# Performance work log

Measured on AMD Instinct MI355X. Metric: run time of the kernel, lower is better.

The kernel has to match this reference:

```python
import jax, jax.numpy as jnp
import numpy as np

N, F, H, C, HX, E = 50000, 256, 128, 16, 64, 500000
TEMP = 1.0


def gcn_conv(x, src, dst, W, b, n):
    # PyG GCNConv: x @ W, add self-loops, sym-normalized scatter-sum src->dst
    xw = x @ W
    idx = jnp.arange(n)
    s = jnp.concatenate([src, idx])
    d = jnp.concatenate([dst, idx])
    deg = jax.ops.segment_sum(jnp.ones_like(s, dtype=xw.dtype), d, num_segments=n)
    dinv = jnp.where(deg > 0, jax.lax.rsqrt(deg), 0.0)
    norm = dinv[s] * dinv[d]
    out = jax.ops.segment_sum(xw[s] * norm[:, None], d, num_segments=n)
    return out + b


def setup_inputs() -> dict:
    key = jax.random.key(0)
    ks = jax.random.split(key, 16)
    x = jax.random.normal(ks[0], (N, F), jnp.float32)
    edge_index = jax.random.randint(ks[1], (2, E), 0, N)
    neg_edge_index = jax.random.randint(ks[2], (2, E), 0, N)
    y = jax.random.randint(ks[3], (N,), 0, C)
    train_mask = jax.random.uniform(ks[4], (N,)) < 0.5
    def lin(k, fi, fo):
        s = 1.0 / np.sqrt(fi)
        return jax.random.uniform(k, (fi, fo), jnp.float32, -s, s)
    W1 = lin(ks[5], F, H); b1 = jnp.zeros((H,), jnp.float32)
    W2 = lin(ks[6], H, C); b2 = jnp.zeros((C,), jnp.float32)
    Wx = lin(ks[7], F, HX); bx = jnp.zeros((HX,), jnp.float32)
    Wd = lin(ks[8], 2 * (HX + C), 1); bd = jnp.zeros((1,), jnp.float32)
    return dict(x=x, edge_index=edge_index, neg_edge_index=neg_edge_index, y=y,
                train_mask=train_mask, W1=W1, b1=b1, W2=W2, b2=b2,
                Wx=Wx, bx=bx, Wd=Wd, bd=bd)


def reference(x, edge_index, neg_edge_index, y, train_mask,
              W1, b1, W2, b2, Wx, bx, Wd, bd):
    n = x.shape[0]
    # GNN encoder p(y|x,G): 2-layer GCN (eval mode -> dropout identity)
    h = jax.nn.relu(gcn_conv(x, edge_index[0], edge_index[1], W1, b1, n))
    logits = gcn_conv(h, edge_index[0], edge_index[1], W2, b2, n) / TEMP
    y_log_prob = jax.nn.log_softmax(logits, axis=-1)
    y_prob = jnp.where(train_mask[:, None],
                       jax.nn.one_hot(y, logits.shape[-1], dtype=logits.dtype),
                       jnp.exp(y_log_prob))
    # node feature encoder
    xe = jax.nn.relu(x @ Wx + bx)
    def decode(ei):
        s, d = ei[0], ei[1]
        feat = jnp.concatenate([xe[s], xe[d], y_prob[s], y_prob[d]], axis=1)
        return feat @ Wd + bd
    e_pred_pos = decode(edge_index)
    e_pred_neg = decode(neg_edge_index)
    return e_pred_pos, e_pred_neg, y_log_prob
```

## Files before the change

kernel.cpp:

```cpp
#include <hip/hip_runtime.h>

typedef unsigned short ushort_t;
typedef __attribute__((ext_vector_type(8))) short short8;
typedef __attribute__((ext_vector_type(4))) float floatx4;

constexpr int F = 256, H = 128, C = 16, HX = 64;
constexpr int NBCOL = H + HX;

__device__ __forceinline__ ushort_t f2bf(float f) {
  unsigned u = __float_as_uint(f);
  u += 0x7fffu + ((u >> 16) & 1u);
  return (ushort_t)(u >> 16);
}
__device__ __forceinline__ float bflo(unsigned u) { return __uint_as_float(u << 16); }
__device__ __forceinline__ float bfhi(unsigned u) { return __uint_as_float(u & 0xffff0000u); }

__global__ void k_pre(const float* __restrict__ x, ushort_t* __restrict__ xb, int total8,
                      const float* __restrict__ W1, const float* __restrict__ Wx,
                      ushort_t* __restrict__ WBt,
                      const int* __restrict__ dst, int* __restrict__ deg, int e,
                      int nbx, int nbw) {
  int b = blockIdx.x;
  if (b < nbx) {
    int i = b * 256 + threadIdx.x;
    if (i >= total8) return;
    const float4* xp = (const float4*)x;
    float4 a = xp[2 * i], bb = xp[2 * i + 1];
    ushort4 lo = make_ushort4(f2bf(a.x), f2bf(a.y), f2bf(a.z), f2bf(a.w));
    ushort4 hi = make_ushort4(f2bf(bb.x), f2bf(bb.y), f2bf(bb.z), f2bf(bb.w));
    ((ushort4*)xb)[2 * i] = lo;
    ((ushort4*)xb)[2 * i + 1] = hi;
  } else if (b < nbx + nbw) {
    int i = (b - nbx) * 256 + threadIdx.x;
    if (i >= NBCOL * F) return;
    int nn = i / F, k = i % F;
    float v = (nn < H) ? W1[k * H + nn] : Wx[k * HX + (nn - H)];
    WBt[nn * F + k] = f2bf(v);
  } else {
    int i = (b - nbx - nbw) * 256 + threadIdx.x;
    if (i < e) atomicAdd(&deg[dst[i]], 1);
  }
}

__global__ void k_scan_a(const int* __restrict__ deg, int* __restrict__ part, int n) {
  __shared__ int sm[256];
  int i = blockIdx.x * 256 + threadIdx.x;
  int v = (i < n) ? deg[i] : 0;
  sm[threadIdx.x] = v;
  __syncthreads();
  for (int s = 128; s > 0; s >>= 1) {
    if (threadIdx.x < s) sm[threadIdx.x] += sm[threadIdx.x + s];
    __syncthreads();
  }
  if (threadIdx.x == 0) part[blockIdx.x] = sm[0];
}

__global__ void k_scan_b(const int* __restrict__ part, int* __restrict__ blockoff, int nparts) {
  __shared__ int sm[256];
  int t = threadIdx.x;
  int v = (t < nparts) ? part[t] : 0;
  sm[t] = v;
  __syncthreads();
  for (int d = 1; d < 256; d <<= 1) {
    int add = (t >= d) ? sm[t - d] : 0;
    __syncthreads();
    sm[t] += add;
    __syncthreads();
  }
  blockoff[t] = sm[t] - v;
}

__global__ void k_scan_c(const int* __restrict__ deg, const int* __restrict__ blockoff,
                         int* __restrict__ row_start, int* __restrict__ cursor,
                         float* __restrict__ dinv, int n, int e) {
  int i = blockIdx.x * 256 + threadIdx.x;
  int lane = threadIdx.x & 63, wid = threadIdx.x >> 6;
  int v = (i < n) ? deg[i] : 0;
  int x = v;
  for (int d = 1; d < 64; d <<= 1) {
    int t = __shfl_up(x, d);
    if (lane >= d) x += t;
  }
  __shared__ int wsum[4], woff[4];
  if (lane == 63) wsum[wid] = x;
  __syncthreads();
  if (threadIdx.x == 0) {
    int s = 0;
    for (int w = 0; w < 4; w++) { woff[w] = s; s += wsum[w]; }
  }
  __syncthreads();
  int excl = x - v + woff[wid] + blockoff[blockIdx.x];
  if (i < n) {
    row_start[i] = excl;
    cursor[i] = excl;
    dinv[i] = rsqrtf((float)(v + 1));
  }
  if (i == 0) row_start[n] = e;
}

__global__ void k_fill(const int* __restrict__ src, const int* __restrict__ dst,
                       const float* __restrict__ dinv, int* __restrict__ cursor,
                       int2* __restrict__ csr8, int e) {
  int i = blockIdx.x * 256 + threadIdx.x;
  if (i < e) {
    int s = src[i];
    int p = atomicAdd(&cursor[dst[i]], 1);
    csr8[p] = make_int2(s, __float_as_int(dinv[s]));
  }
}

__global__ __launch_bounds__(256, 3) void k_gemm1(const ushort_t* __restrict__ xb,
                                                  const ushort_t* __restrict__ WBt,
                                                  const float* __restrict__ bx,
                                                  ushort_t* __restrict__ xw1,
                                                  float* __restrict__ xe,
                                                  int n, int ntiles) {
  int w = threadIdx.x >> 6, lane = threadIdx.x & 63;
  int q = lane >> 4, l15 = lane & 15;
  const short8* bb = (const short8*)WBt;
  short8 bfr[3][8];
#pragma unroll
  for (int t = 0; t < 3; t++)
#pragma unroll
    for (int kk = 0; kk < 8; kk++)
      bfr[t][kk] = bb[(size_t)(w * 48 + t * 16 + l15) * 32 + kk * 4 + q];

  float bxv[3];
#pragma unroll
  for (int t = 0; t < 3; t++) {
    int g = w * 48 + t * 16;
    bxv[t] = (g >= H) ? bx[g - H + l15] : 0.0f;
  }

  for (int tile = blockIdx.x; tile < ntiles; tile += gridDim.x) {
    int row = tile * 16 + l15;
    const short8* arow = (const short8*)(xb + (size_t)min(row, n - 1) * F);
    short8 a[8];
#pragma unroll
    for (int kk = 0; kk < 8; kk++) a[kk] = arow[kk * 4 + q];

    floatx4 acc0 = (floatx4)(0.0f), acc1 = (floatx4)(0.0f), acc2 = (floatx4)(0.0f);
#pragma unroll
    for (int kk = 0; kk < 8; kk++) {
      acc0 = __builtin_amdgcn_mfma_f32_16x16x32_bf16(a[kk], bfr[0][kk], acc0, 0, 0, 0);
      acc1 = __builtin_amdgcn_mfma_f32_16x16x32_bf16(a[kk], bfr[1][kk], acc1, 0, 0, 0);
      acc2 = __builtin_amdgcn_mfma_f32_16x16x32_bf16(a[kk], bfr[2][kk], acc2, 0, 0, 0);
    }

    floatx4 accs[3] = {acc0, acc1, acc2};
    int rbase = tile * 16 + q * 4;
#pragma unroll
    for (int t = 0; t < 3; t++) {
      int g = w * 48 + t * 16;
#pragma unroll
      for (int r = 0; r < 4; r++) {
        int ro = rbase + r;
        if (ro < n) {
          if (g < H) {
            xw1[(size_t)ro * H + g + l15] = f2bf(accs[t][r]);
          } else {
            xe[(size_t)ro * HX + (g - H) + l15] = fmaxf(accs[t][r] + bxv[t], 0.0f);
          }
        }
      }
    }
  }
}

__global__ void k_agg1g2(const ushort_t* __restrict__ xw1, const int* __restrict__ row_start,
                         const int2* __restrict__ csr8, const float* __restrict__ dinv,
                         const float* __restrict__ b1, const float* __restrict__ W2,
                         float* __restrict__ hw2, int n) {
  __shared__ float2 hsm[4][64];
  int wid = threadIdx.x >> 6;
  int v = blockIdx.x * 4 + wid;
  if (v >= n) return;
  int lane = threadIdx.x & 63;
  float dv = dinv[v];
  unsigned sv = ((const unsigned*)(xw1 + (size_t)v * H))[lane];
  float ax = dv * bflo(sv), ay = dv * bfhi(sv);
  int j0 = row_start[v], j1 = row_start[v + 1];
  int j = j0;
  for (; j + 8 <= j1; j += 8) {
    int2 ee[8];
    unsigned rr[8];
#pragma unroll
    for (int u = 0; u < 8; u++) ee[u] = csr8[j + u];
#pragma unroll
    for (int u = 0; u < 8; u++)
      rr[u] = ((const unsigned*)(xw1 + (size_t)ee[u].x * H))[lane];
#pragma unroll
    for (int u = 0; u < 8; u++) {
      float wu = __int_as_float(ee[u].y);
      ax += wu * bflo(rr[u]);
      ay += wu * bfhi(rr[u]);
    }
  }
  for (; j < j1; j++) {
    int2 e0 = csr8[j];
    unsigned r0 = ((const unsigned*)(xw1 + (size_t)e0.x * H))[lane];
    float w0 = __int_as_float(e0.y);
    ax += w0 * bflo(r0);
    ay += w0 * bfhi(r0);
  }
  int c2 = lane * 2;
  float o0 = fmaxf(dv * ax + b1[c2], 0.0f);
  float o1 = fmaxf(dv * ay + b1[c2 + 1], 0.0f);
  hsm[wid][lane] = make_float2(o0, o1);

  int c = lane & 15, g = lane >> 4;
  const float* hrow = (const float*)hsm[wid];
  float p = 0.0f;
#pragma unroll
  for (int jj = 0; jj < 32; jj++)
    p += hrow[g * 32 + jj] * W2[(g * 32 + jj) * C + c];
  p += __shfl_xor(p, 16);
  p += __shfl_xor(p, 32);
  if (g == 0) hw2[(size_t)v * C + c] = p;
}

__global__ void k_agg2ab(const float* __restrict__ hw2, const int* __restrict__ row_start,
                         const int2* __restrict__ csr8, const float* __restrict__ dinv,
                         const float* __restrict__ b2, const int* __restrict__ y,
                         const int* __restrict__ tmask, const float* __restrict__ xe,
                         const float* __restrict__ Wd, float* __restrict__ ylp_out,
                         float* __restrict__ Aarr, float* __restrict__ Barr, int n) {
  int idx = blockIdx.x * 256 + threadIdx.x;
  int node = idx >> 4, c = idx & 15;
  if (node >= n) return;
  float dv = dinv[node];
  float acc = dv * hw2[(size_t)node * C + c];
  int j0 = row_start[node], j1 = row_start[node + 1];
  int j = j0;
  for (; j + 8 <= j1; j += 8) {
    int2 ee[8];
    float rr[8];
#pragma unroll
    for (int u = 0; u < 8; u++) ee[u] = csr8[j + u];
#pragma unroll
    for (int u = 0; u < 8; u++) rr[u] = hw2[(size_t)ee[u].x * C + c];
#pragma unroll
    for (int u = 0; u < 8; u++) acc += __int_as_float(ee[u].y) * rr[u];
  }
  for (; j + 4 <= j1; j += 4) {
    int2 e0 = csr8[j], e1 = csr8[j + 1], e2 = csr8[j + 2], e3 = csr8[j + 3];
    float r0 = hw2[(size_t)e0.x * C + c];
    float r1 = hw2[(size_t)e1.x * C + c];
    float r2 = hw2[(size_t)e2.x * C + c];
    float r3 = hw2[(size_t)e3.x * C + c];
    acc += __int_as_float(e0.y) * r0 + __int_as_float(e1.y) * r1 +
           __int_as_float(e2.y) * r2 + __int_as_float(e3.y) * r3;
  }
  for (; j < j1; j++) {
    int2 e0 = csr8[j];
    acc += __int_as_float(e0.y) * hw2[(size_t)e0.x * C + c];
  }
  float logit = dv * acc + b2[c];
  float m = logit;
  for (int o = 8; o > 0; o >>= 1) m = fmaxf(m, __shfl_xor(m, o, 16));
  float e = expf(logit - m);
  float s16 = e;
  for (int o = 8; o > 0; o >>= 1) s16 += __shfl_xor(s16, o, 16);
  float lp = (logit - m) - logf(s16);
  ylp_out[(size_t)node * C + c] = lp;
  float yp = tmask[node] ? ((y[node] == c) ? 1.0f : 0.0f) : (e / s16);

  float4 xv = *(const float4*)(xe + (size_t)node * HX + c * 4);
  float4 wa = *(const float4*)(Wd + c * 4);
  float4 wb = *(const float4*)(Wd + HX + c * 4);
  float pa = xv.x * wa.x + xv.y * wa.y + xv.z * wa.z + xv.w * wa.w + yp * Wd[2 * HX + c];
  float pb = xv.x * wb.x + xv.y * wb.y + xv.z * wb.z + xv.w * wb.w + yp * Wd[2 * HX + C + c];
  for (int o = 8; o > 0; o >>= 1) {
    pa += __shfl_xor(pa, o, 16);
    pb += __shfl_xor(pb, o, 16);
  }
  if (c == 0) { Aarr[node] = pa; Barr[node] = pb; }
}

__global__ void k_decode(const int* __restrict__ ei, const int* __restrict__ nei,
                         const float* __restrict__ Aarr, const float* __restrict__ Barr,
                         const float* __restrict__ bd, float* __restrict__ out, int e) {
  int i = blockIdx.x * 256 + threadIdx.x;
  if (i >= 2 * e) return;
  float b0 = bd[0];
  if (i < e) {
    int s = ei[i], d = ei[e + i];
    out[i] = Aarr[s] + Barr[d] + b0;
  } else {
    int j = i - e;
    int s = nei[j], d = nei[e + j];
    out[e + j] = Aarr[s] + Barr[d] + b0;
  }
}

extern "C" void kernel_launch(void* const* d_in, const int* in_sizes, int n_in,
                              void* d_out, int out_size, void* d_ws, size_t ws_size,
                              hipStream_t stream) {
  const float* x = (const float*)d_in[0];
  const int* ei = (const int*)d_in[1];
  const int* nei = (const int*)d_in[2];
  const int* y = (const int*)d_in[3];
  const int* tmask = (const int*)d_in[4];
  const float* W1 = (const float*)d_in[5];
  const float* b1 = (const float*)d_in[6];
  const float* W2 = (const float*)d_in[7];
  const float* b2 = (const float*)d_in[8];
  const float* Wx = (const float*)d_in[9];
  const float* bx = (const float*)d_in[10];
  const float* Wd = (const float*)d_in[11];
  const float* bd = (const float*)d_in[12];
  float* out = (float*)d_out;

  int n = in_sizes[3];
  int e = in_sizes[1] / 2;

  char* ws = (char*)d_ws;
  size_t off = 0;
  auto alloc = [&](size_t bytes) -> void* {
    void* p = ws + off;
    off += (bytes + 511) & ~(size_t)511;
    return p;
  };
  int* deg = (int*)alloc((size_t)n * 4);
  ushort_t* xb = (ushort_t*)alloc((size_t)n * F * 2);
  ushort_t* WBt = (ushort_t*)alloc((size_t)NBCOL * F * 2);
  ushort_t* xw1 = (ushort_t*)alloc((size_t)n * H * 2);
  float* xe = (float*)alloc((size_t)n * HX * 4);
  float* hw2 = (float*)alloc((size_t)n * C * 4);
  float* dinv = (float*)alloc((size_t)n * 4);
  int* row_start = (int*)alloc((size_t)(n + 1) * 4);
  int* cursor = (int*)alloc((size_t)n * 4);
  int2* csr8 = (int2*)alloc((size_t)e * 8);
  int* part = (int*)alloc(1024 * 4);
  int* blockoff = (int*)alloc(1024 * 4);
  float* Aarr = (float*)alloc((size_t)n * 4);
  float* Barr = (float*)alloc((size_t)n * 4);

  const int* src = ei;
  const int* dst = ei + e;

  hipMemsetAsync(deg, 0, (size_t)n * 4, stream);

  int total8 = n * F / 8;
  int nbx = (total8 + 255) / 256;
  int nbw = (NBCOL * F + 255) / 256;
  int nbe = (e + 255) / 256;
  k_pre<<<nbx + nbw + nbe, 256, 0, stream>>>(x, xb, total8, W1, Wx, WBt, dst, deg, e,
                                             nbx, nbw);

  int nblk = (n + 255) / 256;
  k_scan_a<<<nblk, 256, 0, stream>>>(deg, part, n);
  k_scan_b<<<1, 256, 0, stream>>>(part, blockoff, nblk);
  k_scan_c<<<nblk, 256, 0, stream>>>(deg, blockoff, row_start, cursor, dinv, n, e);
  k_fill<<<(e + 255) / 256, 256, 0, stream>>>(src, dst, dinv, cursor, csr8, e);

  int ntiles = (n + 15) / 16;
  int ggrid = ntiles < 768 ? ntiles : 768;
  k_gemm1<<<ggrid, 256, 0, stream>>>(xb, WBt, bx, xw1, xe, n, ntiles);
  k_agg1g2<<<(n + 3) / 4, 256, 0, stream>>>(xw1, row_start, csr8, dinv, b1, W2, hw2, n);
  k_agg2ab<<<(n * 16 + 255) / 256, 256, 0, stream>>>(hw2, row_start, csr8, dinv, b2, y,
                                                     tmask, xe, Wd, out + (size_t)2 * e,
                                                     Aarr, Barr, n);
  k_decode<<<(2 * e + 255) / 256, 256, 0, stream>>>(ei, nei, Aarr, Barr, bd, out, e);
}
```

Before: 256.3 us.

## Split GEMM tiles across scan and fill kernels to overlap latency-bound stages

Splits the dense x@[W1|Wx] GEMM into four quarters and fuses each quarter into one of the CSR-building stages (block reduce, single-block scan, final scan, edge fill). Extra blocks in each launch run GEMM tiles while the small latency-bound scan and atomic fill blocks execute, so the GEMM hides their idle time. The fill kernel becomes grid-stride with a fixed block count. The cost is heavier launches with extra register-hungry GEMM blocks, which may slow the scan stages. The GEMM B-fragments are also reloaded four times.

```diff
diff --git a/kernel.cpp b/kernel.cpp
--- a/kernel.cpp
+++ b/kernel.cpp
@@ -6,6 +6,8 @@
 
 constexpr int F = 256, H = 128, C = 16, HX = 64;
 constexpr int NBCOL = H + HX;
+constexpr int GEMM_BLKS = 768;
+constexpr int FILL_BLKS = 512;
 
 __device__ __forceinline__ ushort_t f2bf(float f) {
   unsigned u = __float_as_uint(f);
@@ -42,79 +44,12 @@
   }
 }
 
-__global__ void k_scan_a(const int* __restrict__ deg, int* __restrict__ part, int n) {
-  __shared__ int sm[256];
-  int i = blockIdx.x * 256 + threadIdx.x;
-  int v = (i < n) ? deg[i] : 0;
-  sm[threadIdx.x] = v;
-  __syncthreads();
-  for (int s = 128; s > 0; s >>= 1) {
-    if (threadIdx.x < s) sm[threadIdx.x] += sm[threadIdx.x + s];
-    __syncthreads();
-  }
-  if (threadIdx.x == 0) part[blockIdx.x] = sm[0];
-}
-
-__global__ void k_scan_b(const int* __restrict__ part, int* __restrict__ blockoff, int nparts) {
-  __shared__ int sm[256];
-  int t = threadIdx.x;
-  int v = (t < nparts) ? part[t] : 0;
-  sm[t] = v;
-  __syncthreads();
-  for (int d = 1; d < 256; d <<= 1) {
-    int add = (t >= d) ? sm[t - d] : 0;
-    __syncthreads();
-    sm[t] += add;
-    __syncthreads();
-  }
-  blockoff[t] = sm[t] - v;
-}
-
-__global__ void k_scan_c(const int* __restrict__ deg, const int* __restrict__ blockoff,
-                         int* __restrict__ row_start, int* __restrict__ cursor,
-                         float* __restrict__ dinv, int n, int e) {
-  int i = blockIdx.x * 256 + threadIdx.x;
-  int lane = threadIdx.x & 63, wid = threadIdx.x >> 6;
-  int v = (i < n) ? deg[i] : 0;
-  int x = v;
-  for (int d = 1; d < 64; d <<= 1) {
-    int t = __shfl_up(x, d);
-    if (lane >= d) x += t;
-  }
-  __shared__ int wsum[4], woff[4];
-  if (lane == 63) wsum[wid] = x;
-  __syncthreads();
-  if (threadIdx.x == 0) {
-    int s = 0;
-    for (int w = 0; w < 4; w++) { woff[w] = s; s += wsum[w]; }
-  }
-  __syncthreads();
-  int excl = x - v + woff[wid] + blockoff[blockIdx.x];
-  if (i < n) {
-    row_start[i] = excl;
-    cursor[i] = excl;
-    dinv[i] = rsqrtf((float)(v + 1));
-  }
-  if (i == 0) row_start[n] = e;
-}
-
-__global__ void k_fill(const int* __restrict__ src, const int* __restrict__ dst,
-                       const float* __restrict__ dinv, int* __restrict__ cursor,
-                       int2* __restrict__ csr8, int e) {
-  int i = blockIdx.x * 256 + threadIdx.x;
-  if (i < e) {
-    int s = src[i];
-    int p = atomicAdd(&cursor[dst[i]], 1);
-    csr8[p] = make_int2(s, __float_as_int(dinv[s]));
-  }
-}
-
-__global__ __launch_bounds__(256, 3) void k_gemm1(const ushort_t* __restrict__ xb,
-                                                  const ushort_t* __restrict__ WBt,
-                                                  const float* __restrict__ bx,
-                                                  ushort_t* __restrict__ xw1,
-                                                  float* __restrict__ xe,
-                                                  int n, int ntiles) {
+__device__ __forceinline__ void gemm_tiles(const ushort_t* __restrict__ xb,
+                                           const ushort_t* __restrict__ WBt,
+                                           const float* __restrict__ bx,
+                                           ushort_t* __restrict__ xw1,
+                                           float* __restrict__ xe, int n,
+                                           int t0, int t1, int bidx, int nb) {
   int w = threadIdx.x >> 6, lane = threadIdx.x & 63;
   int q = lane >> 4, l15 = lane & 15;
   const short8* bb = (const short8*)WBt;
@@ -132,7 +67,7 @@
     bxv[t] = (g >= H) ? bx[g - H + l15] : 0.0f;
   }
 
-  for (int tile = blockIdx.x; tile < ntiles; tile += gridDim.x) {
+  for (int tile = t0 + bidx; tile < t1; tile += nb) {
     int row = tile * 16 + l15;
     const short8* arow = (const short8*)(xb + (size_t)min(row, n - 1) * F);
     short8 a[8];
@@ -165,6 +100,116 @@
       }
     }
   }
+}
+
+__global__ __launch_bounds__(256, 3) void k_s2(const int* __restrict__ deg,
+                                               int* __restrict__ part, int n, int nchunk,
+                                               const ushort_t* __restrict__ xb,
+                                               const ushort_t* __restrict__ WBt,
+                                               const float* __restrict__ bx,
+                                               ushort_t* __restrict__ xw1,
+                                               float* __restrict__ xe, int t0, int t1) {
+  if ((int)blockIdx.x < nchunk) {
+    __shared__ int sm[256];
+    int i = blockIdx.x * 256 + threadIdx.x;
+    sm[threadIdx.x] = (i < n) ? deg[i] : 0;
+    __syncthreads();
+    for (int s = 128; s > 0; s >>= 1) {
+      if (threadIdx.x < s) sm[threadIdx.x] += sm[threadIdx.x + s];
+      __syncthreads();
+    }
+    if (threadIdx.x == 0) part[blockIdx.x] = sm[0];
+    return;
+  }
+  gemm_tiles(xb, WBt, bx, xw1, xe, n, t0, t1, blockIdx.x - nchunk, gridDim.x - nchunk);
+}
+
+__global__ __launch_bounds__(256, 3) void k_s3(const int* __restrict__ part,
+                                               int* __restrict__ blockoff, int nparts,
+                                               const ushort_t* __restrict__ xb,
+                                               const ushort_t* __restrict__ WBt,
+                                               const float* __restrict__ bx,
+                                               ushort_t* __restrict__ xw1,
+                                               float* __restrict__ xe, int n,
+                                               int t0, int t1) {
+  if (blockIdx.x == 0) {
+    __shared__ int sm[256];
+    int t = threadIdx.x;
+    int v = (t < nparts) ? part[t] : 0;
+    sm[t] = v;
+    __syncthreads();
+    for (int d = 1; d < 256; d <<= 1) {
+      int add = (t >= d) ? sm[t - d] : 0;
+      __syncthreads();
+      sm[t] += add;
+      __syncthreads();
+    }
+    blockoff[t] = sm[t] - v;
+    return;
+  }
+  gemm_tiles(xb, WBt, bx, xw1, xe, n, t0, t1, blockIdx.x - 1, gridDim.x - 1);
+}
+
+__global__ __launch_bounds__(256, 3) void k_s4(const int* __restrict__ deg,
+                                               const int* __restrict__ blockoff,
+                                               int* __restrict__ row_start,
+                                               int* __restrict__ cursor,
+                                               float* __restrict__ dinv, int n, int e,
+                                               int nchunk,
+                                               const ushort_t* __restrict__ xb,
+                                               const ushort_t* __restrict__ WBt,
+                                               const float* __restrict__ bx,
+                                               ushort_t* __restrict__ xw1,
+                                               float* __restrict__ xe, int t0, int t1) {
+  if ((int)blockIdx.x < nchunk) {
+    __shared__ int wsum[4], woff[4];
+    int i = blockIdx.x * 256 + threadIdx.x;
+    int lane = threadIdx.x & 63, wid = threadIdx.x >> 6;
+    int v = (i < n) ? deg[i] : 0;
+    int xs = v;
+    for (int d = 1; d < 64; d <<= 1) {
+      int t = __shfl_up(xs, d);
+      if (lane >= d) xs += t;
+    }
+    if (lane == 63) wsum[wid] = xs;
+    __syncthreads();
+    if (threadIdx.x == 0) {
+      int s = 0;
+      for (int w = 0; w < 4; w++) { woff[w] = s; s += wsum[w]; }
+    }
+    __syncthreads();
+    int excl = xs - v + woff[wid] + blockoff[blockIdx.x];
+    if (i < n) {
+      row_start[i] = excl;
+      cursor[i] = excl;
+      dinv[i] = rsqrtf((float)(v + 1));
+    }
+    if (i == 0) row_start[n] = e;
+    return;
+  }
+  gemm_tiles(xb, WBt, bx, xw1, xe, n, t0, t1, blockIdx.x - nchunk, gridDim.x - nchunk);
+}
+
+__global__ __launch_bounds__(256, 3) void k_s5(const int* __restrict__ src,
+                                               const int* __restrict__ dst,
+                                               const float* __restrict__ dinv,
+                                               int* __restrict__ cursor,
+                                               int2* __restrict__ csr8, int e,
+                                               const ushort_t* __restrict__ xb,
+                                               const ushort_t* __restrict__ WBt,
+                                               const float* __restrict__ bx,
+                                               ushort_t* __restrict__ xw1,
+                                               float* __restrict__ xe, int n,
+                                               int t0, int t1) {
+  if ((int)blockIdx.x < FILL_BLKS) {
+    for (int i = blockIdx.x * 256 + threadIdx.x; i < e; i += FILL_BLKS * 256) {
+      int s = src[i];
+      int p = atomicAdd(&cursor[dst[i]], 1);
+      csr8[p] = make_int2(s, __float_as_int(dinv[s]));
+    }
+    return;
+  }
+  gemm_tiles(xb, WBt, bx, xw1, xe, n, t0, t1, blockIdx.x - FILL_BLKS, gridDim.x - FILL_BLKS);
 }
 
 __global__ void k_agg1g2(const ushort_t* __restrict__ xw1, const int* __restrict__ row_start,
@@ -348,15 +393,21 @@
   k_pre<<<nbx + nbw + nbe, 256, 0, stream>>>(x, xb, total8, W1, Wx, WBt, dst, deg, e,
                                              nbx, nbw);
 
-  int nblk = (n + 255) / 256;
-  k_scan_a<<<nblk, 256, 0, stream>>>(deg, part, n);
-  k_scan_b<<<1, 256, 0, stream>>>(part, blockoff, nblk);
-  k_scan_c<<<nblk, 256, 0, stream>>>(deg, blockoff, row_start, cursor, dinv, n, e);
-  k_fill<<<(e + 255) / 256, 256, 0, stream>>>(src, dst, dinv, cursor, csr8, e);
-
+  int nchunk = (n + 255) / 256;
   int ntiles = (n + 15) / 16;
-  int ggrid = ntiles < 768 ? ntiles : 768;
-  k_gemm1<<<ggrid, 256, 0, stream>>>(xb, WBt, bx, xw1, xe, n, ntiles);
+  int tq = ntiles / 4;
+  int t1 = tq, t2 = 2 * tq, t3 = 3 * tq;
+
+  k_s2<<<nchunk + GEMM_BLKS, 256, 0, stream>>>(deg, part, n, nchunk,
+                                               xb, WBt, bx, xw1, xe, 0, t1);
+  k_s3<<<1 + GEMM_BLKS, 256, 0, stream>>>(part, blockoff, nchunk,
+                                          xb, WBt, bx, xw1, xe, n, t1, t2);
+  k_s4<<<nchunk + GEMM_BLKS, 256, 0, stream>>>(deg, blockoff, row_start, cursor, dinv,
+                                               n, e, nchunk,
+                                               xb, WBt, bx, xw1, xe, t2, t3);
+  k_s5<<<FILL_BLKS + GEMM_BLKS, 256, 0, stream>>>(src, dst, dinv, cursor, csr8, e,
+                                                  xb, WBt, bx, xw1, xe, n, t3, ntiles);
+
   k_agg1g2<<<(n + 3) / 4, 256, 0, stream>>>(xw1, row_start, csr8, dinv, b1, W2, hw2, n);
   k_agg2ab<<<(n * 16 + 255) / 256, 256, 0, stream>>>(hw2, row_start, csr8, dinv, b2, y,
                                                      tmask, xe, Wd, out + (size_t)2 * e,
```

New measurement: 280.7 us. 9.5% more time.

## Fuse x bf16 conversion into GEMM load and merge scan passes

Applied to the files above, without the earlier changes.

The separate pass that converts x to a bf16 buffer is removed. The GEMM now reads fp32 x directly and converts it to bf16 in registers, which saves writing and re-reading a 25.6MB intermediate. The single-block scan_b kernel is also removed: each scan_c block reduces the preceding partial sums itself, which drops one launch. The costs are doubled read bytes per GEMM tile, higher register pressure (launch bounds lowered to 2), and redundant partial-sum reductions in every block.

```diff
diff --git a/kernel.cpp b/kernel.cpp
--- a/kernel.cpp
+++ b/kernel.cpp
@@ -15,29 +15,19 @@
 __device__ __forceinline__ float bflo(unsigned u) { return __uint_as_float(u << 16); }
 __device__ __forceinline__ float bfhi(unsigned u) { return __uint_as_float(u & 0xffff0000u); }
 
-__global__ void k_pre(const float* __restrict__ x, ushort_t* __restrict__ xb, int total8,
-                      const float* __restrict__ W1, const float* __restrict__ Wx,
+__global__ void k_pre(const float* __restrict__ W1, const float* __restrict__ Wx,
                       ushort_t* __restrict__ WBt,
                       const int* __restrict__ dst, int* __restrict__ deg, int e,
-                      int nbx, int nbw) {
+                      int nbw) {
   int b = blockIdx.x;
-  if (b < nbx) {
+  if (b < nbw) {
     int i = b * 256 + threadIdx.x;
-    if (i >= total8) return;
-    const float4* xp = (const float4*)x;
-    float4 a = xp[2 * i], bb = xp[2 * i + 1];
-    ushort4 lo = make_ushort4(f2bf(a.x), f2bf(a.y), f2bf(a.z), f2bf(a.w));
-    ushort4 hi = make_ushort4(f2bf(bb.x), f2bf(bb.y), f2bf(bb.z), f2bf(bb.w));
-    ((ushort4*)xb)[2 * i] = lo;
-    ((ushort4*)xb)[2 * i + 1] = hi;
-  } else if (b < nbx + nbw) {
-    int i = (b - nbx) * 256 + threadIdx.x;
     if (i >= NBCOL * F) return;
     int nn = i / F, k = i % F;
     float v = (nn < H) ? W1[k * H + nn] : Wx[k * HX + (nn - H)];
     WBt[nn * F + k] = f2bf(v);
   } else {
-    int i = (b - nbx - nbw) * 256 + threadIdx.x;
+    int i = (b - nbw) * 256 + threadIdx.x;
     if (i < e) atomicAdd(&deg[dst[i]], 1);
   }
 }
@@ -55,41 +45,37 @@
   if (threadIdx.x == 0) part[blockIdx.x] = sm[0];
 }
 
-__global__ void k_scan_b(const int* __restrict__ part, int* __restrict__ blockoff, int nparts) {
-  __shared__ int sm[256];
-  int t = threadIdx.x;
-  int v = (t < nparts) ? part[t] : 0;
-  sm[t] = v;
-  __syncthreads();
-  for (int d = 1; d < 256; d <<= 1) {
-    int add = (t >= d) ? sm[t - d] : 0;
-    __syncthreads();
-    sm[t] += add;
-    __syncthreads();
-  }
-  blockoff[t] = sm[t] - v;
-}
-
-__global__ void k_scan_c(const int* __restrict__ deg, const int* __restrict__ blockoff,
+__global__ void k_scan_c(const int* __restrict__ deg, const int* __restrict__ part,
                          int* __restrict__ row_start, int* __restrict__ cursor,
                          float* __restrict__ dinv, int n, int e) {
-  int i = blockIdx.x * 256 + threadIdx.x;
-  int lane = threadIdx.x & 63, wid = threadIdx.x >> 6;
+  __shared__ int psm[256];
+  __shared__ int wsum[4], woff[4];
+  int c = blockIdx.x, t = threadIdx.x;
+  psm[t] = (t < c) ? part[t] : 0;
+  __syncthreads();
+  for (int s = 128; s > 0; s >>= 1) {
+    if (t < s) psm[t] += psm[t + s];
+    __syncthreads();
+  }
+  int blockoff = psm[0];
+  __syncthreads();
+
+  int i = c * 256 + t;
+  int lane = t & 63, wid = t >> 6;
   int v = (i < n) ? deg[i] : 0;
-  int x = v;
+  int xs = v;
   for (int d = 1; d < 64; d <<= 1) {
-    int t = __shfl_up(x, d);
-    if (lane >= d) x += t;
-  }
-  __shared__ int wsum[4], woff[4];
-  if (lane == 63) wsum[wid] = x;
-  __syncthreads();
-  if (threadIdx.x == 0) {
+    int u = __shfl_up(xs, d);
+    if (lane >= d) xs += u;
+  }
+  if (lane == 63) wsum[wid] = xs;
+  __syncthreads();
+  if (t == 0) {
     int s = 0;
     for (int w = 0; w < 4; w++) { woff[w] = s; s += wsum[w]; }
   }
   __syncthreads();
-  int excl = x - v + woff[wid] + blockoff[blockIdx.x];
+  int excl = xs - v + woff[wid] + blockoff;
   if (i < n) {
     row_start[i] = excl;
     cursor[i] = excl;
@@ -109,7 +95,7 @@
   }
 }
 
-__global__ __launch_bounds__(256, 3) void k_gemm1(const ushort_t* __restrict__ xb,
+__global__ __launch_bounds__(256, 2) void k_gemm1(const float* __restrict__ x,
                                                   const ushort_t* __restrict__ WBt,
                                                   const float* __restrict__ bx,
                                                   ushort_t* __restrict__ xw1,
@@ -134,10 +120,22 @@
 
   for (int tile = blockIdx.x; tile < ntiles; tile += gridDim.x) {
     int row = tile * 16 + l15;
-    const short8* arow = (const short8*)(xb + (size_t)min(row, n - 1) * F);
+    const float4* arow = (const float4*)(x + (size_t)min(row, n - 1) * F);
+    float4 f[16];
+#pragma unroll
+    for (int kk = 0; kk < 8; kk++) {
+      f[2 * kk] = arow[kk * 8 + q * 2];
+      f[2 * kk + 1] = arow[kk * 8 + q * 2 + 1];
+    }
     short8 a[8];
 #pragma unroll
-    for (int kk = 0; kk < 8; kk++) a[kk] = arow[kk * 4 + q];
+    for (int kk = 0; kk < 8; kk++) {
+      float4 f0 = f[2 * kk], f1 = f[2 * kk + 1];
+      a[kk][0] = (short)f2bf(f0.x); a[kk][1] = (short)f2bf(f0.y);
+      a[kk][2] = (short)f2bf(f0.z); a[kk][3] = (short)f2bf(f0.w);
+      a[kk][4] = (short)f2bf(f1.x); a[kk][5] = (short)f2bf(f1.y);
+      a[kk][6] = (short)f2bf(f1.z); a[kk][7] = (short)f2bf(f1.w);
+    }
 
     floatx4 acc0 = (floatx4)(0.0f), acc1 = (floatx4)(0.0f), acc2 = (floatx4)(0.0f);
 #pragma unroll
@@ -322,7 +320,6 @@
     return p;
   };
   int* deg = (int*)alloc((size_t)n * 4);
-  ushort_t* xb = (ushort_t*)alloc((size_t)n * F * 2);
   ushort_t* WBt = (ushort_t*)alloc((size_t)NBCOL * F * 2);
   ushort_t* xw1 = (ushort_t*)alloc((size_t)n * H * 2);
   float* xe = (float*)alloc((size_t)n * HX * 4);
@@ -332,7 +329,6 @@
   int* cursor = (int*)alloc((size_t)n * 4);
   int2* csr8 = (int2*)alloc((size_t)e * 8);
   int* part = (int*)alloc(1024 * 4);
-  int* blockoff = (int*)alloc(1024 * 4);
   float* Aarr = (float*)alloc((size_t)n * 4);
   float* Barr = (float*)alloc((size_t)n * 4);
 
@@ -341,22 +337,18 @@
 
   hipMemsetAsync(deg, 0, (size_t)n * 4, stream);
 
-  int total8 = n * F / 8;
-  int nbx = (total8 + 255) / 256;
   int nbw = (NBCOL * F + 255) / 256;
   int nbe = (e + 255) / 256;
-  k_pre<<<nbx + nbw + nbe, 256, 0, stream>>>(x, xb, total8, W1, Wx, WBt, dst, deg, e,
-                                             nbx, nbw);
-
-  int nblk = (n + 255) / 256;
-  k_scan_a<<<nblk, 256, 0, stream>>>(deg, part, n);
-  k_scan_b<<<1, 256, 0, stream>>>(part, blockoff, nblk);
-  k_scan_c<<<nblk, 256, 0, stream>>>(deg, blockoff, row_start, cursor, dinv, n, e);
+  k_pre<<<nbw + nbe, 256, 0, stream>>>(W1, Wx, WBt, dst, deg, e, nbw);
+
+  int nchunk = (n + 255) / 256;
+  k_scan_a<<<nchunk, 256, 0, stream>>>(deg, part, n);
+  k_scan_c<<<nchunk, 256, 0, stream>>>(deg, part, row_start, cursor, dinv, n, e);
   k_fill<<<(e + 255) / 256, 256, 0, stream>>>(src, dst, dinv, cursor, csr8, e);
 
   int ntiles = (n + 15) / 16;
   int ggrid = ntiles < 768 ? ntiles : 768;
-  k_gemm1<<<ggrid, 256, 0, stream>>>(xb, WBt, bx, xw1, xe, n, ntiles);
+  k_gemm1<<<ggrid, 256, 0, stream>>>(x, WBt, bx, xw1, xe, n, ntiles);
   k_agg1g2<<<(n + 3) / 4, 256, 0, stream>>>(xw1, row_start, csr8, dinv, b1, W2, hw2, n);
   k_agg2ab<<<(n * 16 + 255) / 256, 256, 0, stream>>>(hw2, row_start, csr8, dinv, b2, y,
                                                      tmask, xe, Wd, out + (size_t)2 * e,
```

Result: no change. 257.1 us (+0.3%).
